# Kernel optimization log

Hardware: AMD Instinct MI355X
Metric: run time of the kernel (lower is better)

The kernel has to match this reference:

```python
import jax, jax.numpy as jnp
import numpy as np

B, S, T = 64, 128, 32
VOCAB, N_ENT, N_REL = 50000, 200000, 500
IN_DIM, KG_DIM, H, C = 300, 100, 256, 3


def setup_inputs() -> dict:
    key = jax.random.key(0)
    ks = jax.random.split(key, 16)
    inputs = jax.random.randint(ks[0], (B, S), 0, VOCAB)
    head = jax.random.randint(ks[1], (B, S, T, 1), 0, N_ENT)
    tail = jax.random.randint(ks[2], (B, S, T, 1), 0, N_ENT)
    rel = jax.random.randint(ks[3], (B, S, T, 1), 0, N_REL)
    triples = jnp.concatenate([head, tail, rel], axis=-1)  # [B,S,T,3]
    lengths = jax.random.randint(ks[4], (B,), 1, S + 1)
    # values in {-1,0,1}; a token row of all -1 means "no KG triples" (torch.equal branch)
    id2_ids_batch = jax.random.randint(ks[5], (B, S, T), 0, 3) - 1
    s = 0.02
    word_emb = jax.random.normal(ks[6], (VOCAB, IN_DIM)) * s
    ent_emb = jax.random.normal(ks[7], (N_ENT, KG_DIM)) * s
    rel_emb = jax.random.normal(ks[8], (N_REL, KG_DIM)) * s
    W_ent = jax.random.normal(ks[9], (KG_DIM, 2 * KG_DIM)) * s  # entity_transformed (no bias)
    w_ih = jax.random.normal(ks[10], (4 * H, IN_DIM + 2 * KG_DIM)) * s
    w_hh = jax.random.normal(ks[11], (4 * H, H)) * s
    b_ih = jnp.zeros((4 * H,), jnp.float32)
    b_hh = jnp.zeros((4 * H,), jnp.float32)
    W_att = jax.random.normal(ks[12], (1, H)) * s
    b_att = jax.random.normal(ks[13], (1,)) * s
    W_out = jax.random.normal(ks[14], (C, H)) * s
    b_out = jnp.zeros((C,), jnp.float32)
    return dict(inputs=inputs, triples=triples, lengths=lengths, id2_ids_batch=id2_ids_batch,
                word_emb=word_emb, ent_emb=ent_emb, rel_emb=rel_emb, W_ent=W_ent,
                w_ih=w_ih, w_hh=w_hh, b_ih=b_ih, b_hh=b_hh,
                W_att=W_att, b_att=b_att, W_out=W_out, b_out=b_out)


def reference(inputs, triples, lengths, id2_ids_batch, word_emb, ent_emb, rel_emb,
              W_ent, w_ih, w_hh, b_ih, b_hh, W_att, b_att, W_out, b_out):
    x = word_emb[inputs]                                   # [B,S,IN]
    head = ent_emb[triples[..., 0]]                        # [B,S,T,D]
    tail = ent_emb[triples[..., 1]]
    rel = rel_emb[triples[..., 2]]
    head_tail = jnp.concatenate([head, tail], axis=-1)     # [B,S,T,2D]
    # entity_transformed + tanh; relation side only gets tanh (relation_transformed
    # linear is defined but never applied in the original forward — preserved).
    ht_tr = jnp.tanh(jnp.einsum('bstk,dk->bstd', head_tail, W_ent))
    e = jnp.sum(ht_tr * jnp.tanh(rel), axis=-1)            # [B,S,T]
    alpha = jax.nn.softmax(e, axis=-1)                     # softmax over triples
    graph_embed = jnp.einsum('bst,bstk->bsk', alpha, head_tail)  # [B,S,2D]
    valid = jnp.any(id2_ids_batch != -1, axis=-1)          # torch.equal(-1) branches
    graph_embed = jnp.where(valid[..., None], graph_embed, 0.0)
    t = jnp.concatenate([x, graph_embed], axis=-1)         # [B,S,IN+2D]

    def step(carry, xt):
        h, c = carry
        gates = xt @ w_ih.T + h @ w_hh.T + b_ih + b_hh
        i, f, g, o = jnp.split(gates, 4, axis=-1)          # PyTorch gate order
        c = jax.nn.sigmoid(f) * c + jax.nn.sigmoid(i) * jnp.tanh(g)
        h = jax.nn.sigmoid(o) * jnp.tanh(c)
        return (h, c), h

    h0 = jnp.zeros((t.shape[0], w_hh.shape[1]), t.dtype)
    _, hs = jax.lax.scan(step, (h0, h0), jnp.swapaxes(t, 0, 1))  # [S,B,H]
    output = jnp.swapaxes(hs, 0, 1)                               # [B,S,H]
    # pad_packed_sequence -> zeros past each sequence length
    len_mask = jnp.arange(S)[None, :] < lengths[:, None]
    output = output * len_mask[..., None].astype(output.dtype)

    logits = (output @ W_att.T + b_att)[..., 0]            # [B,S]
    mask = (logits != 0).astype(output.dtype)
    # AllenNLP-style last_dim_softmax with mask
    p = jax.nn.softmax(logits * mask, axis=-1) * mask
    p = p / (jnp.sum(p, axis=-1, keepdims=True) + 1e-13)
    enc = jnp.einsum('bs,bsh->bh', p, output)              # [B,H]
    log_probs = jax.nn.log_softmax(enc @ W_out.T + b_out, axis=-1)
    return log_probs, p
```

## Files before the change

kernel.cpp:

```cpp
#include <hip/hip_runtime.h>


typedef unsigned short ushort_t;
typedef unsigned char uchar_t;
typedef __bf16 bf16x8 __attribute__((ext_vector_type(8)));
typedef float f32x4 __attribute__((ext_vector_type(4)));
typedef int i32x4 __attribute__((ext_vector_type(4)));

#define NENT 200000
#define NVOC 50000
#define NREL 500
#define KPAD 512
#define ASW(t, k) ((((t) * 512 + (k) * 2)) ^ (((t) & 7) << 4))

__device__ __forceinline__ float b2f(ushort_t u) {
    return __uint_as_float(((unsigned)u) << 16);
}
__device__ __forceinline__ ushort_t f2b(float f) {
    unsigned u = __float_as_uint(f);
    unsigned r = (u + 0x7FFFu + ((u >> 16) & 1u)) >> 16;
    return (ushort_t)r;
}
__device__ __forceinline__ float sigm(float x) {
    return __builtin_amdgcn_rcpf(1.f + __expf(-x));
}
__device__ __forceinline__ float tanh_fast(float x) {
    float xx = fminf(fmaxf(x, -15.f), 15.f);
    float t = __expf(2.f * xx);
    return 1.f - 2.f * __builtin_amdgcn_rcpf(t + 1.f);
}
__device__ __forceinline__ int iacc(const void* p, long long i, int di) {
    return di ? ((const int*)p)[2 * i] : ((const int*)p)[i];
}

__global__ void k_sentinel(float* __restrict__ out, int n, float val) {
    int i = blockIdx.x * 256 + threadIdx.x;
    if (i < n) out[i] = val;
}

__global__ void k_det(const int* __restrict__ triples, unsigned* __restrict__ dflag) {
    __shared__ int cnt;
    int tid = threadIdx.x;
    if (tid == 0) cnt = 0;
    __syncthreads();
    int nz = 0;
    for (int i = tid; i < 1500; i += 256)
        if (triples[2 * i + 1] != 0) nz++;
    if (nz) atomicAdd(&cnt, nz);
    __syncthreads();
    if (tid == 0) *dflag = (cnt == 0) ? 2u : 0u;
}

__global__ void k_prep(const float* __restrict__ Went, const float* __restrict__ wih,
                       const float* __restrict__ relE,
                       ushort_t* __restrict__ Wb, ushort_t* __restrict__ wihT,
                       float* __restrict__ trelP) {
    int i = blockIdx.x * 256 + threadIdx.x;
    int stride = gridDim.x * 256;
    if (i < 112 * 256) {
        int n = i >> 8, k = i & 255;
        float v = 0.f;
        if (n < 100) {
            if (k < 100) v = Went[n * 200 + k];
            else if (k >= 128 && k < 228) v = Went[n * 200 + 100 + (k - 128)];
        }
        Wb[i] = f2b(v);
    }
    for (int j = i; j < 500 * 128; j += stride) {
        int r_ = j >> 7, d = j & 127;
        if (d < 112) trelP[r_ * 112 + d] = (d < 100) ? tanhf(relE[r_ * 100 + d]) : 0.f;
    }
    for (int j = i; j < 512 * 1024; j += stride) {
        int k = j >> 10, n = j & 1023;
        wihT[j] = (k < 500) ? f2b(wih[(long long)n * 500 + k]) : (ushort_t)0;
    }
}

__global__ void k_prep2(const float* __restrict__ whh, uchar_t* __restrict__ whhI8) {
    int j = blockIdx.x * 256 + threadIdx.x;
    int f = j >> 10, r = j & 1023;
    int lane = r >> 4, jj = r & 15;
    int ntg = f >> 2, kt = f & 3;
    int np = ntg * 16 + (lane & 15);
    int k = kt * 64 + ((lane >> 4) << 4) + jj;
    int u = np >> 2, gg = np & 3;
    int qv = __float2int_rn(whh[(gg * 256 + u) * 256 + k] * 1024.f);
    qv = min(max(qv, -127), 127);
    whhI8[j] = (uchar_t)(qv & 0xFF);
}

__global__ __launch_bounds__(256, 8) void k_graph(const void* __restrict__ inputs,
                                                  const void* __restrict__ triples,
                                                  const void* __restrict__ id2,
                                                  const float* __restrict__ wordE,
                                                  const float* __restrict__ entE,
                                                  const ushort_t* __restrict__ Wb,
                                                  const float* __restrict__ trelP,
                                                  ushort_t* __restrict__ tfeat,
                                                  const unsigned* __restrict__ dflag) {
    int di = ((*dflag) >> 1) & 1;
    int bs = blockIdx.x;
    int tid = threadIdx.x;
    __shared__ __align__(16) uchar_t As[32 * 512];
    __shared__ int hid_sm[32], tl_sm[32], rids[32];
    __shared__ float e_sm[32], alpha[32];
    __shared__ int vflag;
    int wave = tid >> 6, lane = tid & 63;

    if (wave == 0) {
        int idv = -1;
        if (lane < 32) {
            long long base3 = ((long long)bs * 32 + lane) * 3;
            hid_sm[lane] = min(max(iacc(triples, base3, di), 0), NENT - 1);
            tl_sm[lane] = min(max(iacc(triples, base3 + 1, di), 0), NENT - 1);
            rids[lane] = min(max(iacc(triples, base3 + 2, di), 0), NREL - 1);
            idv = iacc(id2, (long long)bs * 32 + lane, di);
        }
        unsigned long long bal = __ballot(idv != -1);
        if (lane == 0) vflag = (bal != 0ULL) ? 1 : 0;
    } else {
        for (int j = tid - 64; j < 32 * 14; j += 192) {
            int t = j / 14, g = j % 14;
            int c = (g < 7) ? (100 + g * 4) : (228 + (g - 7) * 4);
            *(unsigned long long*)&As[ASW(t, c)] = 0ULL;
        }
    }
    __syncthreads();
#pragma unroll 4
    for (int slot = wave; slot < 64; slot += 4) {
        int t = slot & 31;
        const float* src = entE + (long long)((slot < 32) ? hid_sm[t] : tl_sm[t]) * 100;
        int cb = (slot < 32) ? 0 : 128;
        if (lane < 50) {
            float2 v = *(const float2*)(src + 2 * lane);
            unsigned pk = ((unsigned)f2b(v.y) << 16) | (unsigned)f2b(v.x);
            *(unsigned*)&As[ASW(t, cb + 2 * lane)] = pk;
        }
    }
    __syncthreads();
    int m16 = lane & 15, q = lane >> 4;
    if (wave < 2) {
        f32x4 acc[7];
#pragma unroll
        for (int nt = 0; nt < 7; nt++) acc[nt] = {0.f, 0.f, 0.f, 0.f};
#pragma unroll
        for (int ks = 0; ks < 8; ++ks) {
            bf16x8 af = *reinterpret_cast<const bf16x8*>(&As[ASW(wave * 16 + m16, ks * 32 + q * 8)]);
#pragma unroll
            for (int nt = 0; nt < 7; ++nt) {
                bf16x8 bf_ = *reinterpret_cast<const bf16x8*>(&Wb[(nt * 16 + m16) * 256 + ks * 32 + q * 8]);
                acc[nt] = __builtin_amdgcn_mfma_f32_16x16x32_bf16(af, bf_, acc[nt], 0, 0, 0);
            }
        }
#pragma unroll
        for (int rr = 0; rr < 4; ++rr) {
            int m = wave * 16 + q * 4 + rr;
            const float* tr = trelP + rids[m] * 112;
            float s = 0.f;
#pragma unroll
            for (int nt = 0; nt < 7; ++nt) s += tanh_fast(acc[nt][rr]) * tr[nt * 16 + m16];
            s += __shfl_xor(s, 1);
            s += __shfl_xor(s, 2);
            s += __shfl_xor(s, 4);
            s += __shfl_xor(s, 8);
            if (m16 == 0) e_sm[m] = s;
        }
    }
    __syncthreads();
    if (tid < 32) {
        float v = e_sm[tid];
        float mx = v;
        for (int off = 16; off >= 1; off >>= 1) mx = fmaxf(mx, __shfl_xor(mx, off));
        float ex = __expf(v - mx);
        float sm = ex;
        for (int off = 16; off >= 1; off >>= 1) sm += __shfl_xor(sm, off);
        alpha[tid] = ex / sm;
    }
    __syncthreads();
    float scale = vflag ? 1.f : 0.f;
    long long row = (long long)bs * KPAD;
    if (tid < 200) {
        int k = tid;
        int kk = (k < 100) ? k : (k + 28);
        float ge = 0.f;
#pragma unroll 8
        for (int tt = 0; tt < 32; ++tt)
            ge += alpha[tt] * b2f(*(const ushort_t*)&As[ASW(tt, kk)]);
        tfeat[row + 300 + k] = f2b(ge * scale);
    }
    int w = min(max(iacc(inputs, bs, di), 0), NVOC - 1);
    const float* wsrc = wordE + (long long)w * 300;
    if (tid < 150) {
        float2 v = *(const float2*)(wsrc + 2 * tid);
        *(unsigned*)&tfeat[row + 2 * tid] = ((unsigned)f2b(v.y) << 16) | (unsigned)f2b(v.x);
    }
    if (tid < 12) tfeat[row + 500 + tid] = 0;
}

__global__ __launch_bounds__(256) void k_gemm_xw(const ushort_t* __restrict__ A,
                                                 const ushort_t* __restrict__ Bm,
                                                 const float* __restrict__ bih,
                                                 const float* __restrict__ bhh,
                                                 ushort_t* __restrict__ xwB) {
    __shared__ __align__(16) ushort_t As[64 * 32];
    __shared__ __align__(16) ushort_t Bs[64 * 32];
    int tid = threadIdx.x;
    int i0 = blockIdx.x * 64, n0 = blockIdx.y * 64;
    int wave = tid >> 6, lane = tid & 63, m16 = lane & 15, q = lane >> 4;
    f32x4 acc[4];
#pragma unroll
    for (int t = 0; t < 4; t++) acc[t] = {0.f, 0.f, 0.f, 0.f};
    int r = tid >> 2, cq = (tid & 3) * 8;
    int kk = tid >> 3, nn = (tid & 7) * 8;
    for (int kt = 0; kt < 16; ++kt) {
        int k0 = kt * 32;
        {
            const ushort_t* src = A + (i0 + r) * 512 + k0 + cq;
            ushort4 v0 = *(const ushort4*)src;
            ushort4 v1 = *(const ushort4*)(src + 4);
            *(ushort4*)&As[r * 32 + cq] = v0;
            *(ushort4*)&As[r * 32 + cq + 4] = v1;
        }
        {
            const ushort_t* src = Bm + (k0 + kk) * 1024 + n0 + nn;
            ushort4 v0 = *(const ushort4*)(src);
            ushort4 v1 = *(const ushort4*)(src + 4);
            Bs[(nn + 0) * 32 + kk] = v0.x; Bs[(nn + 1) * 32 + kk] = v0.y;
            Bs[(nn + 2) * 32 + kk] = v0.z; Bs[(nn + 3) * 32 + kk] = v0.w;
            Bs[(nn + 4) * 32 + kk] = v1.x; Bs[(nn + 5) * 32 + kk] = v1.y;
            Bs[(nn + 6) * 32 + kk] = v1.z; Bs[(nn + 7) * 32 + kk] = v1.w;
        }
        __syncthreads();
        bf16x8 af = *reinterpret_cast<const bf16x8*>(&As[(wave * 16 + m16) * 32 + q * 8]);
#pragma unroll
        for (int t = 0; t < 4; t++) {
            bf16x8 bf_ = *reinterpret_cast<const bf16x8*>(&Bs[(t * 16 + m16) * 32 + q * 8]);
            acc[t] = __builtin_amdgcn_mfma_f32_16x16x32_bf16(af, bf_, acc[t], 0, 0, 0);
        }
        __syncthreads();
    }
#pragma unroll
    for (int t = 0; t < 4; t++) {
        int n = n0 + t * 16 + m16;
        float bias = bih[n] + bhh[n];
        int ni = ((n & 255) << 2) + (n >> 8);
#pragma unroll
        for (int rr = 0; rr < 4; rr++) {
            int i = i0 + wave * 16 + q * 4 + rr;
            xwB[i * 1024 + ni] = f2b(acc[t][rr] + bias);
        }
    }
}

__global__ __launch_bounds__(512, 2) void k_lstm(const ushort_t* __restrict__ xwB,
                                                 const uchar_t* __restrict__ whhI8,
                                                 const void* __restrict__ lengths,
                                                 ushort_t* __restrict__ hallB,
                                                 const unsigned* __restrict__ dflag) {
    const int LDH = 272;
    int di = ((*dflag) >> 1) & 1;
    int b = blockIdx.x;
    int tid = threadIdx.x;
    int wave = tid >> 6, lane = tid & 63;
    int c16 = lane & 15, q = lane >> 4;
    __shared__ __align__(16) uchar_t hsm[16 * 272];
    __shared__ __align__(16) float gbuf[1024];
    for (int j = tid; j < 16 * 272; j += 512) hsm[j] = 0;
    i32x4 wreg[8][4];
    {
        const uchar_t* wp = whhI8 + (((long long)(wave * 8) * 4) * 64 + lane) * 16;
#pragma unroll
        for (int i = 0; i < 8; ++i)
#pragma unroll
            for (int kt = 0; kt < 4; ++kt)
                wreg[i][kt] = *(const i32x4*)(wp + (((i << 2) + kt) << 10));
    }
    int len = iacc(lengths, b, di);
    int u = tid;
    float cc = 0.f;
    const float S = 1.f / (127.f * 1024.f);
    long long xbase = ((long long)(b * 128) << 10) + ((long long)u << 2);
    ushort4 xv = {0, 0, 0, 0}, xn;
    if (tid < 256) xv = *(const ushort4*)(xwB + xbase);
    __syncthreads();
    for (int s = 0; s < 128; ++s) {
        const uchar_t* hb = &hsm[c16 * LDH];
        i32x4 afr[4];
#pragma unroll
        for (int kt = 0; kt < 4; ++kt)
            afr[kt] = *(const i32x4*)(hb + kt * 64 + q * 16);
        int sn = (s < 127) ? s + 1 : 127;
        if (tid < 256) xn = *(const ushort4*)(xwB + xbase + ((long long)sn << 10));
#pragma unroll
        for (int i = 0; i < 8; ++i) {
            i32x4 a = {0, 0, 0, 0};
#pragma unroll
            for (int kt = 0; kt < 4; ++kt)
                a = __builtin_amdgcn_mfma_i32_16x16x64_i8(afr[kt], wreg[i][kt], a, 0, 0, 0);
            if (q == 0) gbuf[(wave * 8 + i) * 16 + c16] = (float)a[0];
        }
        asm volatile("s_waitcnt lgkmcnt(0)\n\ts_barrier" ::: "memory");
        if (tid < 256) {
            f32x4 gv = *(const f32x4*)&gbuf[u * 4];
            float iv = b2f(xv.x) + gv[0] * S;
            float fv = b2f(xv.y) + gv[1] * S;
            float gg = b2f(xv.z) + gv[2] * S;
            float ov = b2f(xv.w) + gv[3] * S;
            float c = sigm(fv) * cc + sigm(iv) * tanh_fast(gg);
            float h = sigm(ov) * tanh_fast(c);
            cc = c;
            hsm[u] = (uchar_t)(__float2int_rn(h * 127.f) & 0xFF);
            hallB[((long long)(b * 128 + s) << 8) + u] = (s < len) ? f2b(h) : (ushort_t)0;
            xv = xn;
        }
        asm volatile("s_waitcnt lgkmcnt(0)\n\ts_barrier" ::: "memory");
    }
}

__global__ __launch_bounds__(256) void k_att(const ushort_t* __restrict__ hallB,
                                             const float* __restrict__ Watt,
                                             const float* __restrict__ batt,
                                             const float* __restrict__ Wout,
                                             const float* __restrict__ bout,
                                             float* __restrict__ out) {
    int b = blockIdx.x, tid = threadIdx.x;
    __shared__ float waf[256], lg[128], msk[128], ps[128], enc[256], o3[3], red[1];
    waf[tid] = Watt[tid];
    __syncthreads();
    int s = tid >> 1, half = tid & 1;
    const ushort_t* hb = hallB + (b * 128 + s) * 256 + half * 128;
    float part = 0.f;
    for (int j = 0; j < 128; ++j) part += b2f(hb[j]) * waf[half * 128 + j];
    part += __shfl_xor(part, 1);
    if (half == 0) lg[s] = part + batt[0];
    __syncthreads();
    if (tid < 128) {
        float lv = lg[tid];
        float m = (lv != 0.f) ? 1.f : 0.f;
        msk[tid] = m;
        lg[tid] = lv * m;
    }
    __syncthreads();
    if (tid == 0) {
        float mx = -1e30f;
        for (int i = 0; i < 128; ++i) mx = fmaxf(mx, lg[i]);
        red[0] = mx;
    }
    __syncthreads();
    if (tid < 128) ps[tid] = __expf(lg[tid] - red[0]);
    __syncthreads();
    if (tid == 0) {
        float sm = 0.f;
        for (int i = 0; i < 128; ++i) sm += ps[i];
        red[0] = sm;
    }
    __syncthreads();
    if (tid < 128) ps[tid] = ps[tid] / red[0] * msk[tid];
    __syncthreads();
    if (tid == 0) {
        float sm = 0.f;
        for (int i = 0; i < 128; ++i) sm += ps[i];
        red[0] = sm + 1e-13f;
    }
    __syncthreads();
    if (tid < 128) {
        float p = ps[tid] / red[0];
        ps[tid] = p;
        out[192 + b * 128 + tid] = p;
    }
    __syncthreads();
    {
        float ej = 0.f;
        for (int ss = 0; ss < 128; ++ss) ej += ps[ss] * b2f(hallB[(b * 128 + ss) * 256 + tid]);
        enc[tid] = ej;
    }
    __syncthreads();
    if (tid < 3) {
        float a = 0.f;
        for (int j = 0; j < 256; ++j) a += enc[j] * Wout[tid * 256 + j];
        o3[tid] = a + bout[tid];
    }
    __syncthreads();
    if (tid == 0) {
        float m = fmaxf(o3[0], fmaxf(o3[1], o3[2]));
        float l = logf(__expf(o3[0] - m) + __expf(o3[1] - m) + __expf(o3[2] - m)) + m;
        out[b * 3 + 0] = o3[0] - l;
        out[b * 3 + 1] = o3[1] - l;
        out[b * 3 + 2] = o3[2] - l;
    }
}

extern "C" void kernel_launch(void* const* d_in, const int* in_sizes, int n_in,
                              void* d_out, int out_size, void* d_ws, size_t ws_size,
                              hipStream_t stream) {
    float* out = (float*)d_out;
    static const long long EXP[16] = {8192, 786432, 64, 262144, 15000000, 20000000,
                                      50000, 20000, 512000, 262144, 1024, 1024,
                                      256, 1, 768, 3};
    int ob = (out_size + 255) / 256;
    if (n_in != 16 || out_size != 8384) {
        hipLaunchKernelGGL(k_sentinel, dim3(ob), dim3(256), 0, stream, out, out_size, -8192.f);
        return;
    }
    for (int i = 0; i < 16; ++i) {
        if ((long long)in_sizes[i] != EXP[i]) {
            hipLaunchKernelGGL(k_sentinel, dim3(ob), dim3(256), 0, stream, out, out_size,
                               -(4096.f + 32.f * i));
            return;
        }
    }

    const void* inputs = d_in[0];
    const void* triples = d_in[1];
    const void* lengths = d_in[2];
    const void* id2 = d_in[3];
    const float* wordE = (const float*)d_in[4];
    const float* entE = (const float*)d_in[5];
    const float* relE = (const float*)d_in[6];
    const float* Went = (const float*)d_in[7];
    const float* wih = (const float*)d_in[8];
    const float* whh = (const float*)d_in[9];
    const float* bih = (const float*)d_in[10];
    const float* bhh = (const float*)d_in[11];
    const float* Watt = (const float*)d_in[12];
    const float* batt = (const float*)d_in[13];
    const float* Wout = (const float*)d_in[14];
    const float* bout = (const float*)d_in[15];
    char* ws = (char*)d_ws;

    constexpr size_t OFF_XW = 0;
    constexpr size_t OFF_TFEAT = 16777216;
    constexpr size_t OFF_WIHT = 25165824;
    constexpr size_t OFF_WB = 26214400;
    constexpr size_t OFF_FLAGS = 26271744;
    constexpr size_t OFF_TRELP = 26272000;
    constexpr size_t WS_NEEDED = 26496000;

    if (ws_size < WS_NEEDED) {
        hipLaunchKernelGGL(k_sentinel, dim3(ob), dim3(256), 0, stream, out, out_size,
                           -(float)(ws_size >> 20));
        return;
    }

    ushort_t* xwB = (ushort_t*)(ws + OFF_XW);
    ushort_t* tfeat = (ushort_t*)(ws + OFF_TFEAT);
    ushort_t* hallB = (ushort_t*)(ws + OFF_TFEAT);
    ushort_t* wihT = (ushort_t*)(ws + OFF_WIHT);
    uchar_t* whhI8 = (uchar_t*)(ws + OFF_WIHT);
    ushort_t* Wb = (ushort_t*)(ws + OFF_WB);
    unsigned* dflag = (unsigned*)(ws + OFF_FLAGS);
    float* trelP = (float*)(ws + OFF_TRELP);

    hipLaunchKernelGGL(k_det, dim3(1), dim3(256), 0, stream, (const int*)triples, dflag);
    hipLaunchKernelGGL(k_prep, dim3(2048), dim3(256), 0, stream,
                       Went, wih, relE, Wb, wihT, trelP);
    hipLaunchKernelGGL(k_graph, dim3(8192), dim3(256), 0, stream,
                       inputs, triples, id2, wordE, entE, Wb, trelP, tfeat, dflag);
    hipLaunchKernelGGL(k_gemm_xw, dim3(128, 16), dim3(256), 0, stream,
                       tfeat, wihT, bih, bhh, xwB);
    hipLaunchKernelGGL(k_prep2, dim3(1024), dim3(256), 0, stream, whh, whhI8);
    hipLaunchKernelGGL(k_lstm, dim3(64), dim3(512), 0, stream, xwB, whhI8, lengths, hallB, dflag);
    hipLaunchKernelGGL(k_att, dim3(64), dim3(256), 0, stream, hallB, Watt, batt, Wout, bout, out);
}
```

Measured before the change: 493.9 us.

## Quantize entity table to fp8 per call and fuse word gather into xW GEMM

Each call, the prep kernel converts the whole entity embedding table to scaled fp8 e4m3. The graph kernel then gathers 100-byte rows instead of 400-byte fp32 rows and decodes them to bf16 in shared memory. The word embedding gather moves out of the graph kernel into the xW GEMM's A-tile load, so the padded 512-wide feature row is no longer written and read back. The trade is a full-table streaming pass each call, plus reduced precision on entity embeddings that could affect accuracy tolerance.

```diff
diff --git a/kernel.cpp b/kernel.cpp
--- a/kernel.cpp
+++ b/kernel.cpp
@@ -10,7 +10,6 @@
 #define NENT 200000
 #define NVOC 50000
 #define NREL 500
-#define KPAD 512
 #define ASW(t, k) ((((t) * 512 + (k) * 2)) ^ (((t) & 7) << 4))
 
 __device__ __forceinline__ float b2f(ushort_t u) {
@@ -29,6 +28,30 @@
     float t = __expf(2.f * xx);
     return 1.f - 2.f * __builtin_amdgcn_rcpf(t + 1.f);
 }
+__device__ __forceinline__ uchar_t f2fp8(float x) {
+    unsigned s = (__float_as_uint(x) >> 24) & 0x80u;
+    float ax = fabsf(x);
+    if (ax >= 448.f) return (uchar_t)(s | 0x7E);
+    if (ax < 0.015625f) {
+        float t = ax * 512.f + 12582912.f;
+        unsigned q = __float_as_uint(t) & 0xFFu;
+        return (uchar_t)(s | q);
+    }
+    unsigned au = __float_as_uint(ax);
+    unsigned lsb = (au >> 20) & 1u;
+    au += 0x0007FFFFu + lsb;
+    int E = ((int)(au >> 23) & 0xFF) - 127 + 7;
+    unsigned f3 = (au >> 20) & 7u;
+    if (E >= 16) return (uchar_t)(s | 0x7E);
+    return (uchar_t)(s | ((unsigned)E << 3) | f3);
+}
+__device__ __forceinline__ float fp8d64(unsigned b) {
+    unsigned E = (b >> 3) & 15u, m = b & 7u;
+    float nrm = __uint_as_float(((b & 0x80u) << 24) | ((E + 114u) << 23) | (m << 20));
+    float sub = (float)(int)m * 3.0517578125e-05f;
+    if (b & 0x80u) sub = -sub;
+    return E ? nrm : sub;
+}
 __device__ __forceinline__ int iacc(const void* p, long long i, int di) {
     return di ? ((const int*)p)[2 * i] : ((const int*)p)[i];
 }
@@ -52,9 +75,9 @@
 }
 
 __global__ void k_prep(const float* __restrict__ Went, const float* __restrict__ wih,
-                       const float* __restrict__ relE,
+                       const float* __restrict__ relE, const float* __restrict__ entE,
                        ushort_t* __restrict__ Wb, ushort_t* __restrict__ wihT,
-                       float* __restrict__ trelP) {
+                       float* __restrict__ trelP, uchar_t* __restrict__ entE8) {
     int i = blockIdx.x * 256 + threadIdx.x;
     int stride = gridDim.x * 256;
     if (i < 112 * 256) {
@@ -74,6 +97,7 @@
         int k = j >> 10, n = j & 1023;
         wihT[j] = (k < 500) ? f2b(wih[(long long)n * 500 + k]) : (ushort_t)0;
     }
+    for (int j = i; j < 20000000; j += stride) entE8[j] = f2fp8(entE[j] * 64.f);
 }
 
 __global__ void k_prep2(const float* __restrict__ whh, uchar_t* __restrict__ whhI8) {
@@ -92,11 +116,11 @@
 __global__ __launch_bounds__(256, 8) void k_graph(const void* __restrict__ inputs,
                                                   const void* __restrict__ triples,
                                                   const void* __restrict__ id2,
-                                                  const float* __restrict__ wordE,
-                                                  const float* __restrict__ entE,
+                                                  const uchar_t* __restrict__ entE8,
                                                   const ushort_t* __restrict__ Wb,
                                                   const float* __restrict__ trelP,
-                                                  ushort_t* __restrict__ tfeat,
+                                                  ushort_t* __restrict__ graphE,
+                                                  int* __restrict__ tokIds,
                                                   const unsigned* __restrict__ dflag) {
     int di = ((*dflag) >> 1) & 1;
     int bs = blockIdx.x;
@@ -126,15 +150,21 @@
         }
     }
     __syncthreads();
+    int sub = lane >> 5, li = lane & 31;
 #pragma unroll 4
-    for (int slot = wave; slot < 64; slot += 4) {
+    for (int pr = wave * 2; pr < 64; pr += 8) {
+        int slot = pr + sub;
         int t = slot & 31;
-        const float* src = entE + (long long)((slot < 32) ? hid_sm[t] : tl_sm[t]) * 100;
+        const uchar_t* src = entE8 + (long long)((slot < 32) ? hid_sm[t] : tl_sm[t]) * 100;
         int cb = (slot < 32) ? 0 : 128;
-        if (lane < 50) {
-            float2 v = *(const float2*)(src + 2 * lane);
-            unsigned pk = ((unsigned)f2b(v.y) << 16) | (unsigned)f2b(v.x);
-            *(unsigned*)&As[ASW(t, cb + 2 * lane)] = pk;
+        if (li < 25) {
+            unsigned w4 = *(const unsigned*)(src + 4 * li);
+            float f0 = fp8d64(w4 & 255u), f1 = fp8d64((w4 >> 8) & 255u);
+            float f2_ = fp8d64((w4 >> 16) & 255u), f3 = fp8d64(w4 >> 24);
+            unsigned lo = ((unsigned)f2b(f1) << 16) | (unsigned)f2b(f0);
+            unsigned hi = ((unsigned)f2b(f3) << 16) | (unsigned)f2b(f2_);
+            unsigned long long pk = ((unsigned long long)hi << 32) | lo;
+            *(unsigned long long*)&As[ASW(t, cb + 4 * li)] = pk;
         }
     }
     __syncthreads();
@@ -178,7 +208,6 @@
     }
     __syncthreads();
     float scale = vflag ? 1.f : 0.f;
-    long long row = (long long)bs * KPAD;
     if (tid < 200) {
         int k = tid;
         int kk = (k < 100) ? k : (k + 28);
@@ -186,18 +215,14 @@
 #pragma unroll 8
         for (int tt = 0; tt < 32; ++tt)
             ge += alpha[tt] * b2f(*(const ushort_t*)&As[ASW(tt, kk)]);
-        tfeat[row + 300 + k] = f2b(ge * scale);
-    }
-    int w = min(max(iacc(inputs, bs, di), 0), NVOC - 1);
-    const float* wsrc = wordE + (long long)w * 300;
-    if (tid < 150) {
-        float2 v = *(const float2*)(wsrc + 2 * tid);
-        *(unsigned*)&tfeat[row + 2 * tid] = ((unsigned)f2b(v.y) << 16) | (unsigned)f2b(v.x);
-    }
-    if (tid < 12) tfeat[row + 500 + tid] = 0;
-}
-
-__global__ __launch_bounds__(256) void k_gemm_xw(const ushort_t* __restrict__ A,
+        graphE[(long long)bs * 200 + k] = f2b(ge * scale);
+    }
+    if (tid == 0) tokIds[bs] = min(max(iacc(inputs, bs, di), 0), NVOC - 1);
+}
+
+__global__ __launch_bounds__(256) void k_gemm_xw(const ushort_t* __restrict__ graphE,
+                                                 const int* __restrict__ tokIds,
+                                                 const float* __restrict__ wordE,
                                                  const ushort_t* __restrict__ Bm,
                                                  const float* __restrict__ bih,
                                                  const float* __restrict__ bhh,
@@ -212,14 +237,38 @@
     for (int t = 0; t < 4; t++) acc[t] = {0.f, 0.f, 0.f, 0.f};
     int r = tid >> 2, cq = (tid & 3) * 8;
     int kk = tid >> 3, nn = (tid & 7) * 8;
+    int iA = i0 + r;
+    const float* wrow = wordE + (long long)tokIds[iA] * 300;
+    const ushort_t* grow = graphE + (long long)iA * 200;
     for (int kt = 0; kt < 16; ++kt) {
         int k0 = kt * 32;
         {
-            const ushort_t* src = A + (i0 + r) * 512 + k0 + cq;
-            ushort4 v0 = *(const ushort4*)src;
-            ushort4 v1 = *(const ushort4*)(src + 4);
-            *(ushort4*)&As[r * 32 + cq] = v0;
-            *(ushort4*)&As[r * 32 + cq + 4] = v1;
+            int kb = k0 + cq;
+            ushort_t av[8];
+            if (kb + 8 <= 300) {
+                f32x4 w0 = *(const f32x4*)(wrow + kb);
+                f32x4 w1 = *(const f32x4*)(wrow + kb + 4);
+#pragma unroll
+                for (int j = 0; j < 4; ++j) av[j] = f2b(w0[j]);
+#pragma unroll
+                for (int j = 0; j < 4; ++j) av[4 + j] = f2b(w1[j]);
+            } else if (kb >= 304 && kb + 8 <= 500) {
+                ushort4 g0 = *(const ushort4*)(grow + kb - 300);
+                ushort4 g1 = *(const ushort4*)(grow + kb - 296);
+                av[0] = g0.x; av[1] = g0.y; av[2] = g0.z; av[3] = g0.w;
+                av[4] = g1.x; av[5] = g1.y; av[6] = g1.z; av[7] = g1.w;
+            } else {
+#pragma unroll
+                for (int j = 0; j < 8; ++j) {
+                    int k = kb + j;
+                    ushort_t v = 0;
+                    if (k < 300) v = f2b(wrow[k]);
+                    else if (k < 500) v = grow[k - 300];
+                    av[j] = v;
+                }
+            }
+            *(ushort4*)&As[r * 32 + cq] = *(ushort4*)&av[0];
+            *(ushort4*)&As[r * 32 + cq + 4] = *(ushort4*)&av[4];
         }
         {
             const ushort_t* src = Bm + (k0 + kk) * 1024 + n0 + nn;
@@ -428,13 +477,17 @@
     const float* bout = (const float*)d_in[15];
     char* ws = (char*)d_ws;
 
+    constexpr size_t OFF_E8 = 0;
     constexpr size_t OFF_XW = 0;
-    constexpr size_t OFF_TFEAT = 16777216;
-    constexpr size_t OFF_WIHT = 25165824;
-    constexpr size_t OFF_WB = 26214400;
-    constexpr size_t OFF_FLAGS = 26271744;
-    constexpr size_t OFF_TRELP = 26272000;
-    constexpr size_t WS_NEEDED = 26496000;
+    constexpr size_t OFF_GE = 20000000;
+    constexpr size_t OFF_HALL = 20000000;
+    constexpr size_t OFF_WIHT = 23276800;
+    constexpr size_t OFF_TOK = 24325376;
+    constexpr size_t OFF_WHH8 = 24358144;
+    constexpr size_t OFF_WB = 24620288;
+    constexpr size_t OFF_TRELP = 24677632;
+    constexpr size_t OFF_FLAGS = 24901632;
+    constexpr size_t WS_NEEDED = 24901888;
 
     if (ws_size < WS_NEEDED) {
         hipLaunchKernelGGL(k_sentinel, dim3(ob), dim3(256), 0, stream, out, out_size,
@@ -442,22 +495,24 @@
         return;
     }
 
+    uchar_t* entE8 = (uchar_t*)(ws + OFF_E8);
     ushort_t* xwB = (ushort_t*)(ws + OFF_XW);
-    ushort_t* tfeat = (ushort_t*)(ws + OFF_TFEAT);
-    ushort_t* hallB = (ushort_t*)(ws + OFF_TFEAT);
+    ushort_t* graphE = (ushort_t*)(ws + OFF_GE);
+    ushort_t* hallB = (ushort_t*)(ws + OFF_HALL);
     ushort_t* wihT = (ushort_t*)(ws + OFF_WIHT);
-    uchar_t* whhI8 = (uchar_t*)(ws + OFF_WIHT);
+    int* tokIds = (int*)(ws + OFF_TOK);
+    uchar_t* whhI8 = (uchar_t*)(ws + OFF_WHH8);
     ushort_t* Wb = (ushort_t*)(ws + OFF_WB);
     unsigned* dflag = (unsigned*)(ws + OFF_FLAGS);
     float* trelP = (float*)(ws + OFF_TRELP);
 
     hipLaunchKernelGGL(k_det, dim3(1), dim3(256), 0, stream, (const int*)triples, dflag);
     hipLaunchKernelGGL(k_prep, dim3(2048), dim3(256), 0, stream,
-                       Went, wih, relE, Wb, wihT, trelP);
+                       Went, wih, relE, entE, Wb, wihT, trelP, entE8);
     hipLaunchKernelGGL(k_graph, dim3(8192), dim3(256), 0, stream,
-                       inputs, triples, id2, wordE, entE, Wb, trelP, tfeat, dflag);
+                       inputs, triples, id2, entE8, Wb, trelP, graphE, tokIds, dflag);
     hipLaunchKernelGGL(k_gemm_xw, dim3(128, 16), dim3(256), 0, stream,
-                       tfeat, wihT, bih, bhh, xwB);
+                       graphE, tokIds, wordE, wihT, bih, bhh, xwB);
     hipLaunchKernelGGL(k_prep2, dim3(1024), dim3(256), 0, stream, whh, whhI8);
     hipLaunchKernelGGL(k_lstm, dim3(64), dim3(512), 0, stream, xwB, whhI8, lengths, hallB, dflag);
     hipLaunchKernelGGL(k_att, dim3(64), dim3(256), 0, stream, hallB, Watt, batt, Wout, bout, out);
```

Result: no change. 485.8 us (-1.6%).
